# Optimization experiments

Measured on AMD Instinct MI355X. Metric: run time of the kernel, lower is better.

The kernel has to match this reference:

```python
import jax, jax.numpy as jnp
import numpy as np

B, S, F_IN, E = 8, 1024, 256, 512
INNER = 2 * E            # mLSTM proj_factor = 2.0
NH = 4                   # mLSTM num_heads
DH = INNER // NH
KS = 4                   # causal conv1d kernel size
QKV_BS = 4               # qkv_proj_blocksize
NB = INNER // QKV_BS     # number of block-diagonal qkv blocks


def setup_inputs() -> dict:
    key = jax.random.key(0)
    ks = jax.random.split(key, 16)
    g = lambda k, shape, scale: jax.random.normal(k, shape, jnp.float32) * scale
    return {
        "x": g(ks[0], (B, S, F_IN), 1.0),
        "W_in": g(ks[1], (E, F_IN), F_IN ** -0.5),
        "b_in": jnp.zeros((E,), jnp.float32),
        "ln1_w": jnp.ones((E,), jnp.float32),
        "W_up": g(ks[2], (2 * INNER, E), E ** -0.5),
        "conv_w": g(ks[3], (INNER, 1, KS), KS ** -0.5),
        "conv_b": jnp.zeros((INNER,), jnp.float32),
        "Wq": g(ks[4], (NB, QKV_BS, QKV_BS), QKV_BS ** -0.5),
        "Wk": g(ks[5], (NB, QKV_BS, QKV_BS), QKV_BS ** -0.5),
        "Wv": g(ks[6], (NB, QKV_BS, QKV_BS), QKV_BS ** -0.5),
        "W_ig": g(ks[7], (NH, 3 * INNER), (3 * INNER) ** -0.5),
        "b_ig": jnp.zeros((NH,), jnp.float32),
        "W_fg": g(ks[8], (NH, 3 * INNER), (3 * INNER) ** -0.5),
        "b_fg": jnp.linspace(3.0, 6.0, NH, dtype=jnp.float32),  # xlstm fgate bias init
        "mhln_w": jnp.ones((INNER,), jnp.float32),
        "skip": jnp.ones((INNER,), jnp.float32),
        "W_down": g(ks[9], (E, INNER), INNER ** -0.5),
        "ln_post_w": jnp.ones((E,), jnp.float32),
    }


def _ln(h, w, eps=1e-5):
    m = h.mean(-1, keepdims=True)
    v = jnp.mean((h - m) ** 2, axis=-1, keepdims=True)
    return (h - m) * jax.lax.rsqrt(v + eps) * w


def _causal_conv(x, w, b):
    # x: (B,S,C) -> depthwise causal conv, kernel KS, left-pad KS-1
    y = jax.lax.conv_general_dilated(
        x.transpose(0, 2, 1), w, (1,), [(KS - 1, 0)],
        dimension_numbers=("NCH", "OIH", "NCH"), feature_group_count=INNER)
    return y.transpose(0, 2, 1) + b


def _headwise(x, W):
    # block-diagonal linear (LinearHeadwiseExpand, bias=False)
    b, s, _ = x.shape
    xh = x.reshape(b, s, NB, QKV_BS)
    return jnp.einsum("bsni,noi->bsno", xh, W).reshape(b, s, -1)


def reference(x, W_in, b_in, ln1_w, W_up, conv_w, conv_b, Wq, Wk, Wv,
              W_ig, b_ig, W_fg, b_fg, mhln_w, skip, W_down, ln_post_w):
    # input proj (+ dropout = identity in eval)
    xp = x @ W_in.T + b_in                                  # (B,S,E)
    res = xp
    h = _ln(xp, ln1_w)                                      # pre-LN of mLSTM block
    up = h @ W_up.T                                         # (B,S,2*INNER)
    x_m, z = up[..., :INNER], up[..., INNER:]
    xc = jax.nn.silu(_causal_conv(x_m, conv_w, conv_b))     # (B,S,INNER)
    q = _headwise(xc, Wq)
    k = _headwise(xc, Wk)
    v = _headwise(x_m, Wv)
    gate_in = jnp.concatenate([q, k, v], axis=-1)           # (B,S,3*INNER)
    ig = (gate_in @ W_ig.T + b_ig).transpose(0, 2, 1)       # (B,NH,S)
    fg = (gate_in @ W_fg.T + b_fg).transpose(0, 2, 1)       # (B,NH,S)
    to_h = lambda t: t.reshape(B, S, NH, DH).transpose(0, 2, 1, 3)
    qh, kh, vh = to_h(q), to_h(k), to_h(v)                  # (B,NH,S,DH)
    # --- parallel_stabilized_simple mLSTM backend ---
    logf = jax.nn.log_sigmoid(fg)                           # (B,NH,S)
    a = jnp.concatenate([jnp.zeros_like(logf[..., :1]), jnp.cumsum(logf, -1)], -1)
    M = a[..., :, None] - a[..., None, :]                   # (B,NH,S+1,S+1)
    mask = jnp.tril(jnp.ones((S + 1, S + 1), bool))
    logD = jnp.where(mask, M, -jnp.inf)[..., 1:, 1:] + ig[..., None, :]
    maxD = logD.max(-1, keepdims=True)                      # (B,NH,S,1)
    D = jnp.exp(logD - maxD)
    C = jnp.einsum("bnsd,bntd->bnst", qh, kh * (DH ** -0.5)) * D
    n = jnp.maximum(jnp.abs(C.sum(-1, keepdims=True)), jnp.exp(-maxD))
    hh = jnp.einsum("bnst,bntd->bnsd", C / (n + 1e-6), vh)  # (B,NH,S,DH)
    # multi-head layernorm (GroupNorm per head, weight only, bias-free)
    hn = hh.transpose(0, 2, 1, 3)                           # (B,S,NH,DH)
    mu = hn.mean(-1, keepdims=True)
    var = jnp.mean((hn - mu) ** 2, axis=-1, keepdims=True)
    hn = (hn - mu) * jax.lax.rsqrt(var + 1e-5) * mhln_w.reshape(NH, DH)
    hn = hn.reshape(B, S, INNER)
    h_state = (hn + skip * xc) * jax.nn.silu(z)             # learnable skip + output gate
    y = h_state @ W_down.T                                  # (B,S,E)
    out = res + y                                           # residual
    return _ln(out, ln_post_w)                              # post_blocks_norm
```

## Files before the change

kernel.cpp:

```cpp
#include <hip/hip_runtime.h>

#define S_LEN 1024
#define B_SZ 8
#define F_IN_D 256
#define E_DIM 512
#define INNER_D 1024
#define NH_D 4
#define DH_D 256
#define NROW (B_SZ * S_LEN)

typedef _Float16 half8 __attribute__((ext_vector_type(8)));
typedef _Float16 half4_t __attribute__((ext_vector_type(4)));
typedef float v4f __attribute__((ext_vector_type(4)));

__global__ __launch_bounds__(256) void cast4_kernel(
    const float* __restrict__ s0, const float* __restrict__ s1,
    const float* __restrict__ s2, const float* __restrict__ s3,
    _Float16* __restrict__ d0, _Float16* __restrict__ d1,
    _Float16* __restrict__ d2, _Float16* __restrict__ d3,
    int n0, int n1, int n2, int n3)
{
  int i = (blockIdx.x * 256 + threadIdx.x) * 4;
  const float* s; _Float16* d; int off;
  if (i < n0)                { s = s0; d = d0; off = i; }
  else if (i < n0 + n1)      { s = s1; d = d1; off = i - n0; }
  else if (i < n0 + n1 + n2) { s = s2; d = d2; off = i - n0 - n1; }
  else if (i < n0 + n1 + n2 + n3) { s = s3; d = d3; off = i - n0 - n1 - n2; }
  else return;
  float4 v = *(const float4*)(s + off);
  half4_t o = {(_Float16)v.x, (_Float16)v.y, (_Float16)v.z, (_Float16)v.w};
  *(half4_t*)(d + off) = o;
}

#define GBM 128
#define GBN 128
#define GBK 32
#define LDKG (GBK + 8)

__global__ __launch_bounds__(256) void gemm_h16(
    const _Float16* __restrict__ A, const _Float16* __restrict__ B,
    const float* __restrict__ bias, float* __restrict__ C,
    int M, int N, int K)
{
  __shared__ __align__(16) _Float16 As[GBM][LDKG];
  __shared__ __align__(16) _Float16 Bs[GBN][LDKG];
  const int tid = threadIdx.x;
  const int lane = tid & 63, w = tid >> 6;
  const int wr = w >> 1, wc = w & 1;
  const int quad = lane >> 4, l16 = lane & 15;
  const int bm = blockIdx.y * GBM, bn = blockIdx.x * GBN;
  const int srow = tid >> 1;
  const int scol = (tid & 1) * 16;

  v4f acc[4][4];
#pragma unroll
  for (int i = 0; i < 4; ++i)
#pragma unroll
    for (int j = 0; j < 4; ++j) acc[i][j] = (v4f){0.f, 0.f, 0.f, 0.f};

  const _Float16* Ap = A + (size_t)(bm + srow) * K + scol;
  const _Float16* Bp = B + (size_t)(bn + srow) * K + scol;
  half8 a0 = *(const half8*)(Ap);
  half8 a1 = *(const half8*)(Ap + 8);
  half8 b0 = *(const half8*)(Bp);
  half8 b1 = *(const half8*)(Bp + 8);

  for (int k0 = 0; k0 < K; k0 += GBK) {
    __syncthreads();
    *(half8*)(&As[srow][scol]) = a0;
    *(half8*)(&As[srow][scol + 8]) = a1;
    *(half8*)(&Bs[srow][scol]) = b0;
    *(half8*)(&Bs[srow][scol + 8]) = b1;
    __syncthreads();
    if (k0 + GBK < K) {
      const int kn = k0 + GBK;
      a0 = *(const half8*)(Ap + kn);
      a1 = *(const half8*)(Ap + kn + 8);
      b0 = *(const half8*)(Bp + kn);
      b1 = *(const half8*)(Bp + kn + 8);
    }
    half8 af[4], bf[4];
#pragma unroll
    for (int i = 0; i < 4; ++i)
      af[i] = *(const half8*)(&As[wr * 64 + i * 16 + l16][quad * 8]);
#pragma unroll
    for (int j = 0; j < 4; ++j)
      bf[j] = *(const half8*)(&Bs[wc * 64 + j * 16 + l16][quad * 8]);
#pragma unroll
    for (int i = 0; i < 4; ++i)
#pragma unroll
      for (int j = 0; j < 4; ++j)
        acc[i][j] = __builtin_amdgcn_mfma_f32_16x16x32_f16(af[i], bf[j], acc[i][j], 0, 0, 0);
  }

#pragma unroll
  for (int j = 0; j < 4; ++j) {
    const int col = bn + wc * 64 + j * 16 + l16;
    const float bv = bias ? bias[col] : 0.f;
#pragma unroll
    for (int i = 0; i < 4; ++i) {
      const int row0 = bm + wr * 64 + i * 16 + quad * 4;
#pragma unroll
      for (int r = 0; r < 4; ++r)
        C[(size_t)(row0 + r) * N + col] = acc[i][j][r] + bv;
    }
  }
}

__device__ __forceinline__ float block_sum4(float v, float* red, int tid) {
#pragma unroll
  for (int off = 32; off; off >>= 1) v += __shfl_xor(v, off);
  if ((tid & 63) == 0) red[tid >> 6] = v;
  __syncthreads();
  float t = red[0] + red[1] + red[2] + red[3];
  __syncthreads();
  return t;
}

__global__ __launch_bounds__(256) void ln_mul_kernel(
    const float* __restrict__ in, const float* __restrict__ w,
    _Float16* __restrict__ out)
{
  __shared__ float red[4];
  const int row = blockIdx.x;
  const int tid = threadIdx.x;
  const float* p = in + (size_t)row * E_DIM;
  float v0 = p[tid], v1 = p[tid + 256];
  float mean = block_sum4(v0 + v1, red, tid) * (1.f / E_DIM);
  float d0 = v0 - mean, d1 = v1 - mean;
  float var = block_sum4(d0 * d0 + d1 * d1, red, tid) * (1.f / E_DIM);
  float rstd = rsqrtf(var + 1e-5f);
  out[(size_t)row * E_DIM + tid] = (_Float16)(d0 * rstd * w[tid]);
  out[(size_t)row * E_DIM + tid + 256] = (_Float16)(d1 * rstd * w[tid + 256]);
}

__global__ __launch_bounds__(256) void final_ln_kernel(
    const float* __restrict__ res, const float* __restrict__ y,
    const float* __restrict__ w, float* __restrict__ out)
{
  __shared__ float red[4];
  const int row = blockIdx.x;
  const int tid = threadIdx.x;
  const size_t base = (size_t)row * E_DIM;
  float v0 = res[base + tid] + y[base + tid];
  float v1 = res[base + tid + 256] + y[base + tid + 256];
  float mean = block_sum4(v0 + v1, red, tid) * (1.f / E_DIM);
  float d0 = v0 - mean, d1 = v1 - mean;
  float var = block_sum4(d0 * d0 + d1 * d1, red, tid) * (1.f / E_DIM);
  float rstd = rsqrtf(var + 1e-5f);
  out[base + tid] = d0 * rstd * w[tid];
  out[base + tid + 256] = d1 * rstd * w[tid + 256];
}

__global__ __launch_bounds__(256) void chg_kernel(
    const float* __restrict__ up, const float* __restrict__ cw,
    const float* __restrict__ cb,
    const float* __restrict__ Wq, const float* __restrict__ Wk,
    const float* __restrict__ Wv,
    const float* __restrict__ Wig, const float* __restrict__ big,
    const float* __restrict__ Wfg, const float* __restrict__ bfg,
    float* __restrict__ xc, _Float16* __restrict__ qh,
    _Float16* __restrict__ khb, _Float16* __restrict__ vhb,
    float* __restrict__ ig, float* __restrict__ fg)
{
  __shared__ float red[4][8];
  const int row = blockIdx.x;
  const int tid = threadIdx.x;
  const int n = tid;
  const int c = n * 4;
  const int s = row & (S_LEN - 1);
  const float* bp = up + (size_t)row * (2 * INNER_D) + c;
  float4 x0 = *(const float4*)bp;
  float4 x1 = (s >= 1) ? *(const float4*)(bp - 1 * 2 * INNER_D) : (float4){0, 0, 0, 0};
  float4 x2 = (s >= 2) ? *(const float4*)(bp - 2 * 2 * INNER_D) : (float4){0, 0, 0, 0};
  float4 x3 = (s >= 3) ? *(const float4*)(bp - 3 * 2 * INNER_D) : (float4){0, 0, 0, 0};
  float4 cb4 = *(const float4*)(cb + c);
  float xc4[4];
  {
    const float xs3[4] = {x3.x, x3.y, x3.z, x3.w};
    const float xs2[4] = {x2.x, x2.y, x2.z, x2.w};
    const float xs1[4] = {x1.x, x1.y, x1.z, x1.w};
    const float xs0[4] = {x0.x, x0.y, x0.z, x0.w};
    const float cbs[4] = {cb4.x, cb4.y, cb4.z, cb4.w};
#pragma unroll
    for (int j = 0; j < 4; ++j) {
      float4 wch = *(const float4*)(cw + (c + j) * 4);
      float a = cbs[j] + wch.x * xs3[j] + wch.y * xs2[j] + wch.z * xs1[j] + wch.w * xs0[j];
      xc4[j] = a / (1.f + __expf(-a));
    }
  }
  const float* wq = Wq + n * 16;
  const float* wk = Wk + n * 16;
  const float* wv = Wv + n * 16;
  float4 qv, kv, vv;
  qv.x = wq[0] * xc4[0] + wq[1] * xc4[1] + wq[2] * xc4[2] + wq[3] * xc4[3];
  qv.y = wq[4] * xc4[0] + wq[5] * xc4[1] + wq[6] * xc4[2] + wq[7] * xc4[3];
  qv.z = wq[8] * xc4[0] + wq[9] * xc4[1] + wq[10] * xc4[2] + wq[11] * xc4[3];
  qv.w = wq[12] * xc4[0] + wq[13] * xc4[1] + wq[14] * xc4[2] + wq[15] * xc4[3];
  kv.x = wk[0] * xc4[0] + wk[1] * xc4[1] + wk[2] * xc4[2] + wk[3] * xc4[3];
  kv.y = wk[4] * xc4[0] + wk[5] * xc4[1] + wk[6] * xc4[2] + wk[7] * xc4[3];
  kv.z = wk[8] * xc4[0] + wk[9] * xc4[1] + wk[10] * xc4[2] + wk[11] * xc4[3];
  kv.w = wk[12] * xc4[0] + wk[13] * xc4[1] + wk[14] * xc4[2] + wk[15] * xc4[3];
  vv.x = wv[0] * x0.x + wv[1] * x0.y + wv[2] * x0.z + wv[3] * x0.w;
  vv.y = wv[4] * x0.x + wv[5] * x0.y + wv[6] * x0.z + wv[7] * x0.w;
  vv.z = wv[8] * x0.x + wv[9] * x0.y + wv[10] * x0.z + wv[11] * x0.w;
  vv.w = wv[12] * x0.x + wv[13] * x0.y + wv[14] * x0.z + wv[15] * x0.w;
  *(float4*)(xc + (size_t)row * INNER_D + c) = (float4){xc4[0], xc4[1], xc4[2], xc4[3]};
  half4_t qo = {(_Float16)qv.x, (_Float16)qv.y, (_Float16)qv.z, (_Float16)qv.w};
  half4_t ko = {(_Float16)kv.x, (_Float16)kv.y, (_Float16)kv.z, (_Float16)kv.w};
  half4_t vo = {(_Float16)vv.x, (_Float16)vv.y, (_Float16)vv.z, (_Float16)vv.w};
  *(half4_t*)(qh + (size_t)row * INNER_D + c) = qo;
  *(half4_t*)(khb + (size_t)row * INNER_D + c) = ko;
  *(half4_t*)(vhb + (size_t)row * INNER_D + c) = vo;
  float vals[8];
#pragma unroll
  for (int h = 0; h < 4; ++h) {
    const float* wi = Wig + h * 3072 + tid * 4;
    const float* wf = Wfg + h * 3072 + tid * 4;
    float4 w1 = *(const float4*)(wi);
    float4 w2 = *(const float4*)(wi + 1024);
    float4 w3 = *(const float4*)(wi + 2048);
    vals[h] = qv.x * w1.x + qv.y * w1.y + qv.z * w1.z + qv.w * w1.w
            + kv.x * w2.x + kv.y * w2.y + kv.z * w2.z + kv.w * w2.w
            + vv.x * w3.x + vv.y * w3.y + vv.z * w3.z + vv.w * w3.w;
    float4 f1 = *(const float4*)(wf);
    float4 f2 = *(const float4*)(wf + 1024);
    float4 f3 = *(const float4*)(wf + 2048);
    vals[4 + h] = qv.x * f1.x + qv.y * f1.y + qv.z * f1.z + qv.w * f1.w
                + kv.x * f2.x + kv.y * f2.y + kv.z * f2.z + kv.w * f2.w
                + vv.x * f3.x + vv.y * f3.y + vv.z * f3.z + vv.w * f3.w;
  }
  const int lane = tid & 63, wid = tid >> 6;
#pragma unroll
  for (int i = 0; i < 8; ++i) {
    float x = vals[i];
#pragma unroll
    for (int off = 32; off; off >>= 1) x += __shfl_xor(x, off);
    vals[i] = x;
  }
  if (lane == 0) {
#pragma unroll
    for (int i = 0; i < 8; ++i) red[wid][i] = vals[i];
  }
  __syncthreads();
  if (tid < 8) {
    float sm = red[0][tid] + red[1][tid] + red[2][tid] + red[3][tid];
    const int h = tid & 3;
    const int b = row >> 10, ss = row & (S_LEN - 1);
    const size_t oidx = (size_t)(b * NH_D + h) * S_LEN + ss;
    if (tid < 4) ig[oidx] = sm + big[h];
    else         fg[oidx] = sm + bfg[h];
  }
}

__device__ __forceinline__ float logsigf(float x) {
  return fminf(x, 0.f) - log1pf(__expf(-fabsf(x)));
}

__global__ __launch_bounds__(256) void scan_kernel(
    const float* __restrict__ ig, const float* __restrict__ fg,
    float* __restrict__ m_, float* __restrict__ rmax_, float* __restrict__ maxd_,
    float* __restrict__ em_)
{
  __shared__ float sc[256];
  const int bh = blockIdx.x;
  const int tid = threadIdx.x;
  const size_t base = (size_t)bh * S_LEN + tid * 4;
  float4 f4 = *(const float4*)(fg + base);
  float4 i4 = *(const float4*)(ig + base);
  float l0 = logsigf(f4.x), l1 = logsigf(f4.y), l2 = logsigf(f4.z), l3 = logsigf(f4.w);
  float p0 = l0, p1 = p0 + l1, p2 = p1 + l2, p3 = p2 + l3;
  sc[tid] = p3;
  __syncthreads();
  for (int off = 1; off < 256; off <<= 1) {
    float o = (tid >= off) ? sc[tid - off] : 0.f;
    __syncthreads();
    sc[tid] += o;
    __syncthreads();
  }
  float aoff = (tid == 0) ? 0.f : sc[tid - 1];
  __syncthreads();
  float a0 = aoff + p0, a1 = aoff + p1, a2 = aoff + p2, a3 = aoff + p3;
  float m0 = i4.x - a0, m1 = i4.y - a1, m2 = i4.z - a2, m3 = i4.w - a3;
  float x0 = m0, x1 = fmaxf(x0, m1), x2 = fmaxf(x1, m2), x3 = fmaxf(x2, m3);
  sc[tid] = x3;
  __syncthreads();
  for (int off = 1; off < 256; off <<= 1) {
    float o = (tid >= off) ? sc[tid - off] : -1e30f;
    __syncthreads();
    sc[tid] = fmaxf(sc[tid], o);
    __syncthreads();
  }
  float moff = (tid == 0) ? -1e30f : sc[tid - 1];
  float tmax = sc[tid | 15];
  float r0 = fmaxf(moff, x0), r1 = fmaxf(moff, x1), r2 = fmaxf(moff, x2), r3 = fmaxf(moff, x3);
  const float scale = 0.0625f;
  float4 mo = {m0, m1, m2, m3};
  float4 ro = {r0, r1, r2, r3};
  float4 dd = {a0 + r0, a1 + r1, a2 + r2, a3 + r3};
  float4 eo = {scale * __expf(m0 - tmax), scale * __expf(m1 - tmax),
               scale * __expf(m2 - tmax), scale * __expf(m3 - tmax)};
  *(float4*)(m_ + base) = mo;
  *(float4*)(rmax_ + base) = ro;
  *(float4*)(maxd_ + base) = dd;
  *(float4*)(em_ + base) = eo;
}

__global__ __launch_bounds__(256) void vtrans_kernel(
    const _Float16* __restrict__ vb, _Float16* __restrict__ vt)
{
  __shared__ _Float16 tile[64][68];
  const int b = blockIdx.z, dt = blockIdx.x, st = blockIdx.y;
  const int c4 = (threadIdx.x & 15) * 4, rr = threadIdx.x >> 4;
  const int s0 = st * 64, d0 = dt * 64;
#pragma unroll
  for (int i = 0; i < 4; ++i) {
    int r = rr + i * 16;
    half4_t v = *(const half4_t*)(vb + ((size_t)(b * S_LEN + s0 + r)) * INNER_D + d0 + c4);
    tile[r][c4 + 0] = v.x; tile[r][c4 + 1] = v.y;
    tile[r][c4 + 2] = v.z; tile[r][c4 + 3] = v.w;
  }
  __syncthreads();
#pragma unroll
  for (int i = 0; i < 4; ++i) {
    int dd = rr + i * 16;
    half4_t o = {tile[c4 + 0][dd], tile[c4 + 1][dd], tile[c4 + 2][dd], tile[c4 + 3][dd]};
    *(half4_t*)(vt + ((size_t)(b * INNER_D + d0 + dd)) * S_LEN + s0 + c4) = o;
  }
}

#define KP 264
#define VP 72

__global__ __launch_bounds__(256, 2) void attn_blk_kernel(
    const _Float16* __restrict__ qh, const _Float16* __restrict__ khb,
    const _Float16* __restrict__ vt,
    const float* __restrict__ m_, const float* __restrict__ em,
    const float* __restrict__ rmax_, const float* __restrict__ maxd_,
    const float* __restrict__ mhln_w, const float* __restrict__ skip,
    const float* __restrict__ xc, const float* __restrict__ up,
    _Float16* __restrict__ hstate)
{
  __shared__ __align__(16) _Float16 Ks[64][KP];
  __shared__ __align__(16) _Float16 Vs[256][VP];
  __shared__ _Float16 plds[4][16][72];
  const int tid = threadIdx.x;
  const int lane = tid & 63, wid = tid >> 6;
  const int quad = lane >> 4, l16 = lane & 15;
  const int bh = blockIdx.x & 31;
  const int pp = blockIdx.x >> 5;
  const int sblk = 15 - pp;
  const int h = bh & 3, b = bh >> 2;
  _Float16 (*P)[72] = plds[wid];
  const float* rmaxp = rmax_ + (size_t)bh * S_LEN;
  const float* emp = em + (size_t)bh * S_LEN;
  const float* mp = m_ + (size_t)bh * S_LEN;
  const float* maxdp = maxd_ + (size_t)bh * S_LEN;
  const float scale = 0.0625f;

  const _Float16* kg = khb + ((size_t)(b * S_LEN)) * INNER_D + h * DH_D;
  const _Float16* vg = vt + ((size_t)(b * INNER_D + h * DH_D)) * S_LEN;
  const int krow_s = tid >> 5;
  const int kcol_s = (tid & 31) * 8;
  const int vrow_s = tid >> 3;
  const int vcol_s = (tid & 7) * 8;

  const int ntile = sblk + 1;
  const int s0 = sblk * 64 + wid * 16;

  half8 kpre[8], vpre[8];
#pragma unroll
  for (int i = 0; i < 8; ++i) {
    kpre[i] = *(const half8*)(kg + (size_t)(i * 8 + krow_s) * INNER_D + kcol_s);
    vpre[i] = *(const half8*)(vg + (size_t)(i * 32 + vrow_s) * S_LEN + vcol_s);
  }

  half8 qf[8];
  const _Float16* qrow = qh + ((size_t)(b * S_LEN + s0 + l16)) * INNER_D + h * DH_D + quad * 8;
#pragma unroll
  for (int c = 0; c < 8; ++c) qf[c] = *(const half8*)(qrow + c * 32);

  v4f acc[16];
#pragma unroll
  for (int nc = 0; nc < 16; ++nc) acc[nc] = (v4f){0.f, 0.f, 0.f, 0.f};
  float rsum[4] = {0.f, 0.f, 0.f, 0.f};
  float rmax_row[4];
#pragma unroll
  for (int r = 0; r < 4; ++r) rmax_row[r] = rmaxp[s0 + quad * 4 + r];

  for (int tt = 0; tt < ntile; ++tt) {
    const int t0 = tt * 64;
    const bool last = (tt + 1 == ntile);
    __syncthreads();
#pragma unroll
    for (int i = 0; i < 8; ++i) {
      *(half8*)(&Ks[i * 8 + krow_s][kcol_s]) = kpre[i];
      *(half8*)(&Vs[i * 32 + vrow_s][vcol_s]) = vpre[i];
    }
    __syncthreads();
    if (!last) {
      const int tn = t0 + 64;
#pragma unroll
      for (int i = 0; i < 8; ++i) {
        kpre[i] = *(const half8*)(kg + (size_t)(tn + i * 8 + krow_s) * INNER_D + kcol_s);
        vpre[i] = *(const half8*)(vg + (size_t)(i * 32 + vrow_s) * S_LEN + tn + vcol_s);
      }
    }
    const bool diag = last;
    float rowfac[4];
    if (!diag) {
      const float rtile = rmaxp[t0 + 63];
#pragma unroll
      for (int r = 0; r < 4; ++r) rowfac[r] = __expf(rtile - rmax_row[r]);
    }
#pragma unroll
    for (int sub = 0; sub < 4; ++sub) {
      v4f sacc0 = (v4f){0.f, 0.f, 0.f, 0.f};
      v4f sacc1 = (v4f){0.f, 0.f, 0.f, 0.f};
#pragma unroll
      for (int c = 0; c < 4; ++c) {
        half8 kf0 = *(const half8*)(&Ks[sub * 16 + l16][c * 32 + quad * 8]);
        half8 kf1 = *(const half8*)(&Ks[sub * 16 + l16][(c + 4) * 32 + quad * 8]);
        sacc0 = __builtin_amdgcn_mfma_f32_16x16x32_f16(qf[c], kf0, sacc0, 0, 0, 0);
        sacc1 = __builtin_amdgcn_mfma_f32_16x16x32_f16(qf[c + 4], kf1, sacc1, 0, 0, 0);
      }
      v4f sacc = sacc0 + sacc1;
      const int t = t0 + sub * 16 + l16;
      if (diag) {
        const float mt = mp[t];
#pragma unroll
        for (int r = 0; r < 4; ++r) {
          const int srow = s0 + quad * 4 + r;
          float cc = (t <= srow) ? sacc[r] * scale * __expf(mt - rmax_row[r]) : 0.f;
          rsum[r] += cc;
          P[quad * 4 + r][sub * 16 + l16] = (_Float16)cc;
        }
      } else {
        const float emv = emp[t];
#pragma unroll
        for (int r = 0; r < 4; ++r) {
          float cc = sacc[r] * emv * rowfac[r];
          rsum[r] += cc;
          P[quad * 4 + r][sub * 16 + l16] = (_Float16)cc;
        }
      }
    }
    asm volatile("s_waitcnt lgkmcnt(0)" ::: "memory");
    half8 pf0 = *(const half8*)(&P[l16][quad * 8]);
    half8 pf1 = *(const half8*)(&P[l16][32 + quad * 8]);
#pragma unroll
    for (int nc = 0; nc < 16; ++nc) {
      half8 vf0 = *(const half8*)(&Vs[nc * 16 + l16][quad * 8]);
      half8 vf1 = *(const half8*)(&Vs[nc * 16 + l16][32 + quad * 8]);
      acc[nc] = __builtin_amdgcn_mfma_f32_16x16x32_f16(pf0, vf0, acc[nc], 0, 0, 0);
      acc[nc] = __builtin_amdgcn_mfma_f32_16x16x32_f16(pf1, vf1, acc[nc], 0, 0, 0);
    }
  }

  float inv[4];
#pragma unroll
  for (int r = 0; r < 4; ++r) {
    float rs = rsum[r];
    rs += __shfl_xor(rs, 1); rs += __shfl_xor(rs, 2);
    rs += __shfl_xor(rs, 4); rs += __shfl_xor(rs, 8);
    float md = maxdp[s0 + quad * 4 + r];
    float n = fmaxf(fabsf(rs), __expf(-md));
    inv[r] = 1.f / (n + 1e-6f);
  }
#pragma unroll
  for (int nc = 0; nc < 16; ++nc) {
#pragma unroll
    for (int r = 0; r < 4; ++r) acc[nc][r] *= inv[r];
  }
  float mean[4], rstd[4];
#pragma unroll
  for (int r = 0; r < 4; ++r) {
    float sm = 0.f;
#pragma unroll
    for (int nc = 0; nc < 16; ++nc) sm += acc[nc][r];
    sm += __shfl_xor(sm, 1); sm += __shfl_xor(sm, 2);
    sm += __shfl_xor(sm, 4); sm += __shfl_xor(sm, 8);
    mean[r] = sm * (1.f / DH_D);
  }
#pragma unroll
  for (int r = 0; r < 4; ++r) {
    float sq = 0.f;
#pragma unroll
    for (int nc = 0; nc < 16; ++nc) { float d = acc[nc][r] - mean[r]; sq += d * d; }
    sq += __shfl_xor(sq, 1); sq += __shfl_xor(sq, 2);
    sq += __shfl_xor(sq, 4); sq += __shfl_xor(sq, 8);
    rstd[r] = rsqrtf(sq * (1.f / DH_D) + 1e-5f);
  }
#pragma unroll
  for (int nc = 0; nc < 16; ++nc) {
    const int d = h * DH_D + nc * 16 + l16;
    const float w = mhln_w[d];
    const float sk = skip[d];
#pragma unroll
    for (int r = 0; r < 4; ++r) {
      const size_t row = (size_t)(b * S_LEN + s0 + quad * 4 + r);
      float xcv = xc[row * INNER_D + d];
      float zv = up[row * 2 * INNER_D + INNER_D + d];
      float sz = zv / (1.f + __expf(-zv));
      float o = ((acc[nc][r] - mean[r]) * rstd[r] * w + sk * xcv) * sz;
      hstate[row * INNER_D + d] = (_Float16)o;
    }
  }
}

extern "C" void kernel_launch(void* const* d_in, const int* in_sizes, int n_in,
                              void* d_out, int out_size, void* d_ws, size_t ws_size,
                              hipStream_t stream)
{
  const float* x      = (const float*)d_in[0];
  const float* W_in   = (const float*)d_in[1];
  const float* b_in   = (const float*)d_in[2];
  const float* ln1_w  = (const float*)d_in[3];
  const float* W_up   = (const float*)d_in[4];
  const float* conv_w = (const float*)d_in[5];
  const float* conv_b = (const float*)d_in[6];
  const float* Wq     = (const float*)d_in[7];
  const float* Wk     = (const float*)d_in[8];
  const float* Wv     = (const float*)d_in[9];
  const float* W_ig   = (const float*)d_in[10];
  const float* b_ig   = (const float*)d_in[11];
  const float* W_fg   = (const float*)d_in[12];
  const float* b_fg   = (const float*)d_in[13];
  const float* mhln_w = (const float*)d_in[14];
  const float* skip   = (const float*)d_in[15];
  const float* W_down = (const float*)d_in[16];
  const float* ln_post_w = (const float*)d_in[17];
  float* out = (float*)d_out;

  float* ws = (float*)d_ws;
  size_t o = 0;
  float* xp     = ws + o; o += (size_t)NROW * E_DIM;
  float* hbuf   = ws + o; o += (size_t)NROW * E_DIM;
  float* up     = ws + o; o += (size_t)NROW * 2 * INNER_D;
  float* xc     = ws + o; o += (size_t)NROW * INNER_D;
  _Float16* h16 = (_Float16*)(ws + o);
  size_t ho = 0;
  _Float16* xh      = h16 + ho; ho += (size_t)NROW * F_IN_D;
  _Float16* WinH    = h16 + ho; ho += (size_t)E_DIM * F_IN_D;
  _Float16* WupH    = h16 + ho; ho += (size_t)2 * INNER_D * E_DIM;
  _Float16* WdownH  = h16 + ho; ho += (size_t)E_DIM * INNER_D;
  _Float16* hh      = h16 + ho; ho += (size_t)NROW * E_DIM;
  _Float16* qh      = h16 + ho; ho += (size_t)NROW * INNER_D;
  _Float16* khb     = h16 + ho; ho += (size_t)NROW * INNER_D;
  _Float16* vhb     = h16 + ho; ho += (size_t)NROW * INNER_D;
  _Float16* vtb     = h16 + ho; ho += (size_t)NROW * INNER_D;
  _Float16* hstateH = h16 + ho; ho += (size_t)NROW * INNER_D;

  const int GSZ = B_SZ * NH_D * S_LEN;
  float* igb   = hbuf;
  float* fgb   = hbuf + GSZ;
  float* mb    = hbuf + 2 * GSZ;
  float* rmaxb = hbuf + 3 * GSZ;
  float* maxdb = hbuf + 4 * GSZ;
  float* emb   = hbuf + 5 * GSZ;
  float* yb    = hbuf;

  dim3 blk(256);
  const int nx = NROW * F_IN_D, nwi = E_DIM * F_IN_D,
            nwu = 2 * INNER_D * E_DIM, nwd = E_DIM * INNER_D;
  const int ntot = nx + nwi + nwu + nwd;
  cast4_kernel<<<(ntot / 4 + 255) / 256, blk, 0, stream>>>(
      x, W_in, W_up, W_down, xh, WinH, WupH, WdownH, nx, nwi, nwu, nwd);
  gemm_h16<<<dim3(E_DIM / GBN, NROW / GBM), blk, 0, stream>>>(
      xh, WinH, b_in, xp, NROW, E_DIM, F_IN_D);
  ln_mul_kernel<<<NROW, blk, 0, stream>>>(xp, ln1_w, hh);
  gemm_h16<<<dim3(2 * INNER_D / GBN, NROW / GBM), blk, 0, stream>>>(
      hh, WupH, nullptr, up, NROW, 2 * INNER_D, E_DIM);
  chg_kernel<<<NROW, blk, 0, stream>>>(
      up, conv_w, conv_b, Wq, Wk, Wv, W_ig, b_ig, W_fg, b_fg,
      xc, qh, khb, vhb, igb, fgb);
  scan_kernel<<<B_SZ * NH_D, blk, 0, stream>>>(igb, fgb, mb, rmaxb, maxdb, emb);
  vtrans_kernel<<<dim3(16, 16, 8), blk, 0, stream>>>(vhb, vtb);
  attn_blk_kernel<<<512, blk, 0, stream>>>(
      qh, khb, vtb, mb, emb, rmaxb, maxdb, mhln_w, skip, xc, up, hstateH);
  gemm_h16<<<dim3(E_DIM / GBN, NROW / GBM), blk, 0, stream>>>(
      hstateH, WdownH, nullptr, yb, NROW, E_DIM, INNER_D);
  final_ln_kernel<<<NROW, blk, 0, stream>>>(xp, yb, ln_post_w, out);
}
```

Measured before the change: 327.7 us.

## Emit fp16 up-projection with fused silu(z), process four rows per conv block

A dedicated up-projection GEMM writes the x half as fp16 and the z half as precomputed fp16 silu(z), replacing the fp32 'up' buffer. The conv/gate kernel now handles four consecutive rows per block, reusing overlapping conv taps and the per-thread weights, and stores xc in fp16. The attention epilogue reads the fp16 xc and silu(z) directly. The aim is to roughly halve intermediate memory traffic and cut redundant loads, at the cost of extra fp16 rounding on xc and the gate.

```diff
diff --git a/kernel.cpp b/kernel.cpp
--- a/kernel.cpp
+++ b/kernel.cpp
@@ -103,6 +103,84 @@
 #pragma unroll
       for (int r = 0; r < 4; ++r)
         C[(size_t)(row0 + r) * N + col] = acc[i][j][r] + bv;
+    }
+  }
+}
+
+__global__ __launch_bounds__(256) void gemm_h16_up(
+    const _Float16* __restrict__ A, const _Float16* __restrict__ B,
+    _Float16* __restrict__ xmh, _Float16* __restrict__ szb,
+    int M, int N, int K)
+{
+  __shared__ __align__(16) _Float16 As[GBM][LDKG];
+  __shared__ __align__(16) _Float16 Bs[GBN][LDKG];
+  const int tid = threadIdx.x;
+  const int lane = tid & 63, w = tid >> 6;
+  const int wr = w >> 1, wc = w & 1;
+  const int quad = lane >> 4, l16 = lane & 15;
+  const int bm = blockIdx.y * GBM, bn = blockIdx.x * GBN;
+  const int srow = tid >> 1;
+  const int scol = (tid & 1) * 16;
+
+  v4f acc[4][4];
+#pragma unroll
+  for (int i = 0; i < 4; ++i)
+#pragma unroll
+    for (int j = 0; j < 4; ++j) acc[i][j] = (v4f){0.f, 0.f, 0.f, 0.f};
+
+  const _Float16* Ap = A + (size_t)(bm + srow) * K + scol;
+  const _Float16* Bp = B + (size_t)(bn + srow) * K + scol;
+  half8 a0 = *(const half8*)(Ap);
+  half8 a1 = *(const half8*)(Ap + 8);
+  half8 b0 = *(const half8*)(Bp);
+  half8 b1 = *(const half8*)(Bp + 8);
+
+  for (int k0 = 0; k0 < K; k0 += GBK) {
+    __syncthreads();
+    *(half8*)(&As[srow][scol]) = a0;
+    *(half8*)(&As[srow][scol + 8]) = a1;
+    *(half8*)(&Bs[srow][scol]) = b0;
+    *(half8*)(&Bs[srow][scol + 8]) = b1;
+    __syncthreads();
+    if (k0 + GBK < K) {
+      const int kn = k0 + GBK;
+      a0 = *(const half8*)(Ap + kn);
+      a1 = *(const half8*)(Ap + kn + 8);
+      b0 = *(const half8*)(Bp + kn);
+      b1 = *(const half8*)(Bp + kn + 8);
+    }
+    half8 af[4], bf[4];
+#pragma unroll
+    for (int i = 0; i < 4; ++i)
+      af[i] = *(const half8*)(&As[wr * 64 + i * 16 + l16][quad * 8]);
+#pragma unroll
+    for (int j = 0; j < 4; ++j)
+      bf[j] = *(const half8*)(&Bs[wc * 64 + j * 16 + l16][quad * 8]);
+#pragma unroll
+    for (int i = 0; i < 4; ++i)
+#pragma unroll
+      for (int j = 0; j < 4; ++j)
+        acc[i][j] = __builtin_amdgcn_mfma_f32_16x16x32_f16(af[i], bf[j], acc[i][j], 0, 0, 0);
+  }
+
+  const bool zhalf = (bn >= INNER_D);
+#pragma unroll
+  for (int j = 0; j < 4; ++j) {
+    const int col = bn + wc * 64 + j * 16 + l16;
+    const int colm = col & (INNER_D - 1);
+#pragma unroll
+    for (int i = 0; i < 4; ++i) {
+      const int row0 = bm + wr * 64 + i * 16 + quad * 4;
+#pragma unroll
+      for (int r = 0; r < 4; ++r) {
+        float a = acc[i][j][r];
+        if (zhalf) {
+          float s = a / (1.f + __expf(-a));
+          szb[(size_t)(row0 + r) * INNER_D + colm] = (_Float16)s;
+        } else {
+          xmh[(size_t)(row0 + r) * INNER_D + colm] = (_Float16)a;
+        }
+      }
     }
   }
 }
@@ -153,86 +231,101 @@
 }
 
 __global__ __launch_bounds__(256) void chg_kernel(
-    const float* __restrict__ up, const float* __restrict__ cw,
+    const _Float16* __restrict__ xm, const float* __restrict__ cw,
     const float* __restrict__ cb,
     const float* __restrict__ Wq, const float* __restrict__ Wk,
     const float* __restrict__ Wv,
     const float* __restrict__ Wig, const float* __restrict__ big,
     const float* __restrict__ Wfg, const float* __restrict__ bfg,
-    float* __restrict__ xc, _Float16* __restrict__ qh,
+    _Float16* __restrict__ xch, _Float16* __restrict__ qh,
     _Float16* __restrict__ khb, _Float16* __restrict__ vhb,
     float* __restrict__ ig, float* __restrict__ fg)
 {
-  __shared__ float red[4][8];
-  const int row = blockIdx.x;
+  __shared__ float red[4][32];
   const int tid = threadIdx.x;
-  const int n = tid;
-  const int c = n * 4;
-  const int s = row & (S_LEN - 1);
-  const float* bp = up + (size_t)row * (2 * INNER_D) + c;
-  float4 x0 = *(const float4*)bp;
-  float4 x1 = (s >= 1) ? *(const float4*)(bp - 1 * 2 * INNER_D) : (float4){0, 0, 0, 0};
-  float4 x2 = (s >= 2) ? *(const float4*)(bp - 2 * 2 * INNER_D) : (float4){0, 0, 0, 0};
-  float4 x3 = (s >= 3) ? *(const float4*)(bp - 3 * 2 * INNER_D) : (float4){0, 0, 0, 0};
+  const int lane = tid & 63, wid = tid >> 6;
+  const int row0 = blockIdx.x * 4;
+  const int sl0 = row0 & (S_LEN - 1);
+  const int c = tid * 4;
+
+  float t[7][4];
+#pragma unroll
+  for (int j = 0; j < 7; ++j) {
+    const int off = j - 3;
+    if (sl0 + off < 0) {
+      t[j][0] = t[j][1] = t[j][2] = t[j][3] = 0.f;
+    } else {
+      half4_t hv = *(const half4_t*)(xm + (size_t)(row0 + off) * INNER_D + c);
+      t[j][0] = (float)hv.x; t[j][1] = (float)hv.y;
+      t[j][2] = (float)hv.z; t[j][3] = (float)hv.w;
+    }
+  }
+  float wct[4][4];
+#pragma unroll
+  for (int j = 0; j < 4; ++j) {
+    float4 wc4 = *(const float4*)(cw + (c + j) * 4);
+    wct[j][0] = wc4.x; wct[j][1] = wc4.y; wct[j][2] = wc4.z; wct[j][3] = wc4.w;
+  }
   float4 cb4 = *(const float4*)(cb + c);
-  float xc4[4];
-  {
-    const float xs3[4] = {x3.x, x3.y, x3.z, x3.w};
-    const float xs2[4] = {x2.x, x2.y, x2.z, x2.w};
-    const float xs1[4] = {x1.x, x1.y, x1.z, x1.w};
-    const float xs0[4] = {x0.x, x0.y, x0.z, x0.w};
-    const float cbs[4] = {cb4.x, cb4.y, cb4.z, cb4.w};
+  const float cbs[4] = {cb4.x, cb4.y, cb4.z, cb4.w};
+  float wqm[16], wkm[16], wvm[16];
+#pragma unroll
+  for (int i = 0; i < 4; ++i) {
+    float4 a = *(const float4*)(Wq + tid * 16 + i * 4);
+    float4 bq = *(const float4*)(Wk + tid * 16 + i * 4);
+    float4 cq = *(const float4*)(Wv + tid * 16 + i * 4);
+    wqm[i * 4] = a.x; wqm[i * 4 + 1] = a.y; wqm[i * 4 + 2] = a.z; wqm[i * 4 + 3] = a.w;
+    wkm[i * 4] = bq.x; wkm[i * 4 + 1] = bq.y; wkm[i * 4 + 2] = bq.z; wkm[i * 4 + 3] = bq.w;
+    wvm[i * 4] = cq.x; wvm[i * 4 + 1] = cq.y; wvm[i * 4 + 2] = cq.z; wvm[i * 4 + 3] = cq.w;
+  }
+
+  float q4[4][4], k4[4][4], v4m[4][4];
+#pragma unroll
+  for (int r = 0; r < 4; ++r) {
+    float xc4[4];
 #pragma unroll
     for (int j = 0; j < 4; ++j) {
-      float4 wch = *(const float4*)(cw + (c + j) * 4);
-      float a = cbs[j] + wch.x * xs3[j] + wch.y * xs2[j] + wch.z * xs1[j] + wch.w * xs0[j];
+      float a = cbs[j] + wct[j][0] * t[r][j] + wct[j][1] * t[r + 1][j]
+                       + wct[j][2] * t[r + 2][j] + wct[j][3] * t[r + 3][j];
       xc4[j] = a / (1.f + __expf(-a));
     }
-  }
-  const float* wq = Wq + n * 16;
-  const float* wk = Wk + n * 16;
-  const float* wv = Wv + n * 16;
-  float4 qv, kv, vv;
-  qv.x = wq[0] * xc4[0] + wq[1] * xc4[1] + wq[2] * xc4[2] + wq[3] * xc4[3];
-  qv.y = wq[4] * xc4[0] + wq[5] * xc4[1] + wq[6] * xc4[2] + wq[7] * xc4[3];
-  qv.z = wq[8] * xc4[0] + wq[9] * xc4[1] + wq[10] * xc4[2] + wq[11] * xc4[3];
-  qv.w = wq[12] * xc4[0] + wq[13] * xc4[1] + wq[14] * xc4[2] + wq[15] * xc4[3];
-  kv.x = wk[0] * xc4[0] + wk[1] * xc4[1] + wk[2] * xc4[2] + wk[3] * xc4[3];
-  kv.y = wk[4] * xc4[0] + wk[5] * xc4[1] + wk[6] * xc4[2] + wk[7] * xc4[3];
-  kv.z = wk[8] * xc4[0] + wk[9] * xc4[1] + wk[10] * xc4[2] + wk[11] * xc4[3];
-  kv.w = wk[12] * xc4[0] + wk[13] * xc4[1] + wk[14] * xc4[2] + wk[15] * xc4[3];
-  vv.x = wv[0] * x0.x + wv[1] * x0.y + wv[2] * x0.z + wv[3] * x0.w;
-  vv.y = wv[4] * x0.x + wv[5] * x0.y + wv[6] * x0.z + wv[7] * x0.w;
-  vv.z = wv[8] * x0.x + wv[9] * x0.y + wv[10] * x0.z + wv[11] * x0.w;
-  vv.w = wv[12] * x0.x + wv[13] * x0.y + wv[14] * x0.z + wv[15] * x0.w;
-  *(float4*)(xc + (size_t)row * INNER_D + c) = (float4){xc4[0], xc4[1], xc4[2], xc4[3]};
-  half4_t qo = {(_Float16)qv.x, (_Float16)qv.y, (_Float16)qv.z, (_Float16)qv.w};
-  half4_t ko = {(_Float16)kv.x, (_Float16)kv.y, (_Float16)kv.z, (_Float16)kv.w};
-  half4_t vo = {(_Float16)vv.x, (_Float16)vv.y, (_Float16)vv.z, (_Float16)vv.w};
-  *(half4_t*)(qh + (size_t)row * INNER_D + c) = qo;
-  *(half4_t*)(khb + (size_t)row * INNER_D + c) = ko;
-  *(half4_t*)(vhb + (size_t)row * INNER_D + c) = vo;
-  float vals[8];
-#pragma unroll
-  for (int h = 0; h < 4; ++h) {
-    const float* wi = Wig + h * 3072 + tid * 4;
-    const float* wf = Wfg + h * 3072 + tid * 4;
-    float4 w1 = *(const float4*)(wi);
-    float4 w2 = *(const float4*)(wi + 1024);
-    float4 w3 = *(const float4*)(wi + 2048);
-    vals[h] = qv.x * w1.x + qv.y * w1.y + qv.z * w1.z + qv.w * w1.w
-            + kv.x * w2.x + kv.y * w2.y + kv.z * w2.z + kv.w * w2.w
-            + vv.x * w3.x + vv.y * w3.y + vv.z * w3.z + vv.w * w3.w;
-    float4 f1 = *(const float4*)(wf);
-    float4 f2 = *(const float4*)(wf + 1024);
-    float4 f3 = *(const float4*)(wf + 2048);
-    vals[4 + h] = qv.x * f1.x + qv.y * f1.y + qv.z * f1.z + qv.w * f1.w
-                + kv.x * f2.x + kv.y * f2.y + kv.z * f2.z + kv.w * f2.w
-                + vv.x * f3.x + vv.y * f3.y + vv.z * f3.z + vv.w * f3.w;
-  }
-  const int lane = tid & 63, wid = tid >> 6;
-#pragma unroll
-  for (int i = 0; i < 8; ++i) {
+#pragma unroll
+    for (int i = 0; i < 4; ++i) {
+      q4[r][i] = wqm[i * 4] * xc4[0] + wqm[i * 4 + 1] * xc4[1]
+               + wqm[i * 4 + 2] * xc4[2] + wqm[i * 4 + 3] * xc4[3];
+      k4[r][i] = wkm[i * 4] * xc4[0] + wkm[i * 4 + 1] * xc4[1]
+               + wkm[i * 4 + 2] * xc4[2] + wkm[i * 4 + 3] * xc4[3];
+      v4m[r][i] = wvm[i * 4] * t[r + 3][0] + wvm[i * 4 + 1] * t[r + 3][1]
+                + wvm[i * 4 + 2] * t[r + 3][2] + wvm[i * 4 + 3] * t[r + 3][3];
+    }
+    const size_t base = (size_t)(row0 + r) * INNER_D + c;
+    half4_t xo = {(_Float16)xc4[0], (_Float16)xc4[1], (_Float16)xc4[2], (_Float16)xc4[3]};
+    half4_t qo = {(_Float16)q4[r][0], (_Float16)q4[r][1], (_Float16)q4[r][2], (_Float16)q4[r][3]};
+    half4_t ko = {(_Float16)k4[r][0], (_Float16)k4[r][1], (_Float16)k4[r][2], (_Float16)k4[r][3]};
+    half4_t vo = {(_Float16)v4m[r][0], (_Float16)v4m[r][1], (_Float16)v4m[r][2], (_Float16)v4m[r][3]};
+    *(half4_t*)(xch + base) = xo;
+    *(half4_t*)(qh + base) = qo;
+    *(half4_t*)(khb + base) = ko;
+    *(half4_t*)(vhb + base) = vo;
+  }
+
+  float vals[32];
+#pragma unroll
+  for (int g = 0; g < 8; ++g) {
+    const float* wb = (g < 4 ? Wig : Wfg) + (g & 3) * 3072 + c;
+    float4 w1 = *(const float4*)(wb);
+    float4 w2 = *(const float4*)(wb + 1024);
+    float4 w3 = *(const float4*)(wb + 2048);
+#pragma unroll
+    for (int r = 0; r < 4; ++r) {
+      vals[g * 4 + r] =
+          q4[r][0] * w1.x + q4[r][1] * w1.y + q4[r][2] * w1.z + q4[r][3] * w1.w
+        + k4[r][0] * w2.x + k4[r][1] * w2.y + k4[r][2] * w2.z + k4[r][3] * w2.w
+        + v4m[r][0] * w3.x + v4m[r][1] * w3.y + v4m[r][2] * w3.z + v4m[r][3] * w3.w;
+    }
+  }
+#pragma unroll
+  for (int i = 0; i < 32; ++i) {
     float x = vals[i];
 #pragma unroll
     for (int off = 32; off; off >>= 1) x += __shfl_xor(x, off);
@@ -240,16 +333,17 @@
   }
   if (lane == 0) {
 #pragma unroll
-    for (int i = 0; i < 8; ++i) red[wid][i] = vals[i];
+    for (int i = 0; i < 32; ++i) red[wid][i] = vals[i];
   }
   __syncthreads();
-  if (tid < 8) {
+  if (tid < 32) {
     float sm = red[0][tid] + red[1][tid] + red[2][tid] + red[3][tid];
-    const int h = tid & 3;
-    const int b = row >> 10, ss = row & (S_LEN - 1);
-    const size_t oidx = (size_t)(b * NH_D + h) * S_LEN + ss;
-    if (tid < 4) ig[oidx] = sm + big[h];
-    else         fg[oidx] = sm + bfg[h];
+    const int g = tid >> 2, r = tid & 3;
+    const int h = g & 3;
+    const int b = row0 >> 10;
+    const size_t oidx = (size_t)(b * NH_D + h) * S_LEN + sl0 + r;
+    if (g < 4) ig[oidx] = sm + big[h];
+    else       fg[oidx] = sm + bfg[h];
   }
 }
 
@@ -338,7 +432,7 @@
     const float* __restrict__ m_, const float* __restrict__ em,
     const float* __restrict__ rmax_, const float* __restrict__ maxd_,
     const float* __restrict__ mhln_w, const float* __restrict__ skip,
-    const float* __restrict__ xc, const float* __restrict__ up,
+    const _Float16* __restrict__ xch, const _Float16* __restrict__ szb,
     _Float16* __restrict__ hstate)
 {
   __shared__ __align__(16) _Float16 Ks[64][KP];
@@ -499,9 +593,8 @@
 #pragma unroll
     for (int r = 0; r < 4; ++r) {
       const size_t row = (size_t)(b * S_LEN + s0 + quad * 4 + r);
-      float xcv = xc[row * INNER_D + d];
-      float zv = up[row * 2 * INNER_D + INNER_D + d];
-      float sz = zv / (1.f + __expf(-zv));
+      float xcv = (float)xch[row * INNER_D + d];
+      float sz = (float)szb[row * INNER_D + d];
       float o = ((acc[nc][r] - mean[r]) * rstd[r] * w + sk * xcv) * sz;
       hstate[row * INNER_D + d] = (_Float16)o;
     }
@@ -536,8 +629,6 @@
   size_t o = 0;
   float* xp     = ws + o; o += (size_t)NROW * E_DIM;
   float* hbuf   = ws + o; o += (size_t)NROW * E_DIM;
-  float* up     = ws + o; o += (size_t)NROW * 2 * INNER_D;
-  float* xc     = ws + o; o += (size_t)NROW * INNER_D;
   _Float16* h16 = (_Float16*)(ws + o);
   size_t ho = 0;
   _Float16* xh      = h16 + ho; ho += (size_t)NROW * F_IN_D;
@@ -545,6 +636,9 @@
   _Float16* WupH    = h16 + ho; ho += (size_t)2 * INNER_D * E_DIM;
   _Float16* WdownH  = h16 + ho; ho += (size_t)E_DIM * INNER_D;
   _Float16* hh      = h16 + ho; ho += (size_t)NROW * E_DIM;
+  _Float16* xmh     = h16 + ho; ho += (size_t)NROW * INNER_D;
+  _Float16* szb     = h16 + ho; ho += (size_t)NROW * INNER_D;
+  _Float16* xch     = h16 + ho; ho += (size_t)NROW * INNER_D;
   _Float16* qh      = h16 + ho; ho += (size_t)NROW * INNER_D;
   _Float16* khb     = h16 + ho; ho += (size_t)NROW * INNER_D;
   _Float16* vhb     = h16 + ho; ho += (size_t)NROW * INNER_D;
@@ -569,15 +663,15 @@
   gemm_h16<<<dim3(E_DIM / GBN, NROW / GBM), blk, 0, stream>>>(
       xh, WinH, b_in, xp, NROW, E_DIM, F_IN_D);
   ln_mul_kernel<<<NROW, blk, 0, stream>>>(xp, ln1_w, hh);
-  gemm_h16<<<dim3(2 * INNER_D / GBN, NROW / GBM), blk, 0, stream>>>(
-      hh, WupH, nullptr, up, NROW, 2 * INNER_D, E_DIM);
-  chg_kernel<<<NROW, blk, 0, stream>>>(
-      up, conv_w, conv_b, Wq, Wk, Wv, W_ig, b_ig, W_fg, b_fg,
-      xc, qh, khb, vhb, igb, fgb);
+  gemm_h16_up<<<dim3(2 * INNER_D / GBN, NROW / GBM), blk, 0, stream>>>(
+      hh, WupH, xmh, szb, NROW, 2 * INNER_D, E_DIM);
+  chg_kernel<<<NROW / 4, blk, 0, stream>>>(
+      xmh, conv_w, conv_b, Wq, Wk, Wv, W_ig, b_ig, W_fg, b_fg,
+      xch, qh, khb, vhb, igb, fgb);
   scan_kernel<<<B_SZ * NH_D, blk, 0, stream>>>(igb, fgb, mb, rmaxb, maxdb, emb);
   vtrans_kernel<<<dim3(16, 16, 8), blk, 0, stream>>>(vhb, vtb);
   attn_blk_kernel<<<512, blk, 0, stream>>>(
-      qh, khb, vtb, mb, emb, rmaxb, maxdb, mhln_w, skip, xc, up, hstateH);
+      qh, khb, vtb, mb, emb, rmaxb, maxdb, mhln_w, skip, xch, szb, hstateH);
   gemm_h16<<<dim3(E_DIM / GBN, NROW / GBM), blk, 0, stream>>>(
       hstateH, WdownH, nullptr, yb, NROW, E_DIM, INNER_D);
   final_ln_kernel<<<NROW, blk, 0, stream>>>(xp, yb, ln_post_w, out);
```

Measured after the change: 286.4 us. 1.14x faster.
